# Optimization experiments

Measured on AMD Instinct MI355X. Metric: run time of the kernel, lower is better.

## Reference

```python
import jax, jax.numpy as jnp
import numpy as np

N = 20000; F = 2000; H1 = 256; H2 = 64; E = 320000
BN_EPS = 1e-5


def setup_inputs() -> dict:
    key = jax.random.key(0)
    ks = jax.random.split(key, 32)
    def w(k, shape, fan_in):
        return jax.random.normal(k, shape, jnp.float32) * (1.0 / np.sqrt(fan_in))
    inp = {
        'x': jax.random.normal(ks[0], (N, F), jnp.float32),
        's_src': jax.random.randint(ks[1], (E,), 0, N, jnp.int32),
        's_dst': jax.random.randint(ks[2], (E,), 0, N, jnp.int32),
        's_w': jax.random.uniform(ks[3], (E,), jnp.float32),
        'f_src': jax.random.randint(ks[4], (E,), 0, N, jnp.int32),
        'f_dst': jax.random.randint(ks[5], (E,), 0, N, jnp.int32),
        'f_w': jax.random.uniform(ks[6], (E,), jnp.float32),
        'Ws1': w(ks[7], (F, H1), F), 'bs1': jnp.zeros((H1,), jnp.float32),
        'Ws2': w(ks[8], (H1, H2), H1), 'bs2': jnp.zeros((H2,), jnp.float32),
        'Wf1': w(ks[9], (F, H1), F), 'bf1': jnp.zeros((H1,), jnp.float32),
        'Wf2': w(ks[10], (H1, H2), H1), 'bf2': jnp.zeros((H2,), jnp.float32),
        'Wc1': w(ks[11], (F, H1), F), 'bc1': jnp.zeros((H1,), jnp.float32),
        'Wc2': w(ks[12], (H1, H2), H1), 'bc2': jnp.zeros((H2,), jnp.float32),
        'Wa1': w(ks[13], (H2, 16), H2), 'ba1': jnp.zeros((16,), jnp.float32),
        'Wa2': w(ks[14], (16, 1), 16),
        'Wm': w(ks[15], (H2, H2), H2), 'bm': jnp.zeros((H2,), jnp.float32),
        'Wd': w(ks[16], (H2, H1), H2), 'bd': jnp.zeros((H1,), jnp.float32),
        'bn_g': jnp.ones((H1,), jnp.float32), 'bn_b': jnp.zeros((H1,), jnp.float32),
        'bn_rm': jnp.zeros((H1,), jnp.float32), 'bn_rv': jnp.ones((H1,), jnp.float32),
        'Wpi': w(ks[17], (H1, F), H1), 'bpi': jnp.zeros((F,), jnp.float32),
        'Wdp': w(ks[18], (H1, F), H1), 'bdp': jnp.zeros((F,), jnp.float32),
        'Wmu': w(ks[19], (H1, F), H1), 'bmu': jnp.zeros((F,), jnp.float32),
    }
    return inp


def _spmm(src, dst, ew, h):
    # out[i] = sum over edges (j->i) ew * h[j]   (sparse adj @ dense)
    return jax.ops.segment_sum(h[src] * ew[:, None], dst, num_segments=N)


def _gcn(x, src, dst, ew, W1, b1, W2, b2):
    h = jax.nn.relu(_spmm(src, dst, ew, x @ W1) + b1)
    # dropout p=0 in eval -> identity
    return _spmm(src, dst, ew, h @ W2) + b2


def reference(x, s_src, s_dst, s_w, f_src, f_dst, f_w,
              Ws1, bs1, Ws2, bs2, Wf1, bf1, Wf2, bf2, Wc1, bc1, Wc2, bc2,
              Wa1, ba1, Wa2, Wm, bm, Wd, bd, bn_g, bn_b, bn_rm, bn_rv,
              Wpi, bpi, Wdp, bdp, Wmu, bmu):
    emb1 = _gcn(x, s_src, s_dst, s_w, Ws1, bs1, Ws2, bs2)   # SGCN on sadj
    emb2 = _gcn(x, f_src, f_dst, f_w, Wf1, bf1, Wf2, bf2)   # FGCN on fadj
    # CGCN applied to both graphs (com_comb is computed but unused in original)
    _ = _gcn(x, s_src, s_dst, s_w, Wc1, bc1, Wc2, bc2)
    _ = _gcn(x, f_src, f_dst, f_w, Wc1, bc1, Wc2, bc2)
    z = jnp.stack([emb1, emb2], axis=1)                     # [N, 2, H2]
    att_logits = jnp.tanh(z @ Wa1 + ba1) @ Wa2              # [N, 2, 1]
    beta = jax.nn.softmax(att_logits, axis=1)
    emb = (beta * z).sum(axis=1)                            # [N, H2]
    emb = emb @ Wm + bm                                     # MLP
    # ZINB decoder: Linear -> BatchNorm1d (eval) -> ReLU
    h = emb @ Wd + bd
    h = (h - bn_rm) * jax.lax.rsqrt(bn_rv + BN_EPS) * bn_g + bn_b
    h = jax.nn.relu(h)
    pi = jax.nn.sigmoid(h @ Wpi + bpi)
    disp = jnp.clip(jax.nn.softplus(h @ Wdp + bdp), 1e-4, 1e4)
    mean = jax.nn.sigmoid(h @ Wmu + bmu)
    return (emb1, emb2, emb, pi, disp, mean)
```

## Files before the change

### kernel.cpp

```cpp
#include <hip/hip_runtime.h>


typedef unsigned short bfu;

__device__ __forceinline__ float b2f(bfu u) {
    return __uint_as_float(((unsigned)u) << 16);
}
__device__ __forceinline__ bfu f2b(float f) {
    unsigned u = __float_as_uint(f);
    return (bfu)((u + 0x7FFFu + ((u >> 16) & 1u)) >> 16);
}
__device__ __forceinline__ float ldm(const void* p, size_t i, int bf) {
    return bf ? b2f(((const bfu*)p)[i]) : ((const float*)p)[i];
}
__device__ __forceinline__ void stm(void* p, size_t i, float v, int bf) {
    if (bf) ((bfu*)p)[i] = f2b(v);
    else    ((float*)p)[i] = v;
}

__global__ void detect_dtype_k(const unsigned* __restrict__ sw, int* __restrict__ flag) {
    __shared__ int cnt;
    if (threadIdx.x == 0) cnt = 0;
    __syncthreads();
    unsigned w = sw[threadIdx.x];
    if ((w & 0xFFFFu) >= 0x3F80u) atomicAdd(&cnt, 1);
    __syncthreads();
    if (threadIdx.x == 0) *flag = (cnt < 25) ? 1 : 0;
}

enum { EPI_F32 = 0, EPI_SIG = 1, EPI_SP = 2 };

template <bool AGLB, int EPI>
__global__ __launch_bounds__(256) void gemm_tiled(
    const void* __restrict__ A, const void* __restrict__ B,
    const void* __restrict__ bias,
    float* __restrict__ Cf, void* __restrict__ Cb, size_t cb_off,
    int M, int K, int Nn, const int* __restrict__ flag)
{
    __shared__ __align__(16) float As[16][68];
    __shared__ __align__(16) float Bs[16][68];

    const int bf = *flag;
    const int t = threadIdx.x;
    const int bm0 = blockIdx.x * 64, bn0 = blockIdx.y * 64;
    const int tx = t & 15, ty = t >> 4;

    const int am = t >> 2;
    const int ak = (t & 3) * 4;
    const int gm = bm0 + am;
    const bool arow = gm < M;
    const int bk = t >> 4;
    const int bn = (t & 15) * 4;
    const bool bcol = (bn0 + bn + 3) < Nn;

    float acc[4][4] = {};

    for (int k0 = 0; k0 < K; k0 += 16) {
        float av0 = 0.f, av1 = 0.f, av2 = 0.f, av3 = 0.f;
        float bv0 = 0.f, bv1 = 0.f, bv2 = 0.f, bv3 = 0.f;
        if (arow) {
            size_t off = (size_t)gm * K + k0 + ak;
            if (AGLB && bf) {
                ushort4 v = *(const ushort4*)((const bfu*)A + off);
                av0 = b2f(v.x); av1 = b2f(v.y); av2 = b2f(v.z); av3 = b2f(v.w);
            } else {
                float4 v = *(const float4*)((const float*)A + off);
                av0 = v.x; av1 = v.y; av2 = v.z; av3 = v.w;
            }
        }
        if (bcol) {
            size_t off = (size_t)(k0 + bk) * Nn + bn0 + bn;
            if (bf) {
                ushort4 v = *(const ushort4*)((const bfu*)B + off);
                bv0 = b2f(v.x); bv1 = b2f(v.y); bv2 = b2f(v.z); bv3 = b2f(v.w);
            } else {
                float4 v = *(const float4*)((const float*)B + off);
                bv0 = v.x; bv1 = v.y; bv2 = v.z; bv3 = v.w;
            }
        }

        __syncthreads();
        As[ak + 0][am] = av0; As[ak + 1][am] = av1;
        As[ak + 2][am] = av2; As[ak + 3][am] = av3;
        *(float4*)&Bs[bk][bn] = make_float4(bv0, bv1, bv2, bv3);
        __syncthreads();

        #pragma unroll
        for (int k = 0; k < 16; k++) {
            float4 a4 = *(const float4*)&As[k][ty * 4];
            float4 b4 = *(const float4*)&Bs[k][tx * 4];
            float aa[4] = {a4.x, a4.y, a4.z, a4.w};
            float bb[4] = {b4.x, b4.y, b4.z, b4.w};
            #pragma unroll
            for (int i = 0; i < 4; i++)
                #pragma unroll
                for (int j = 0; j < 4; j++)
                    acc[i][j] += aa[i] * bb[j];
        }
    }

    #pragma unroll
    for (int i = 0; i < 4; i++) {
        int row = bm0 + ty * 4 + i;
        if (row >= M) continue;
        #pragma unroll
        for (int j = 0; j < 4; j++) {
            int col = bn0 + tx * 4 + j;
            if (col >= Nn) continue;
            float v = acc[i][j];
            if constexpr (EPI == EPI_F32) {
                Cf[(size_t)row * Nn + col] = v;
            } else if constexpr (EPI == EPI_SIG) {
                v += ldm(bias, col, bf);
                v = 1.f / (1.f + __expf(-v));
                stm(Cb, cb_off + (size_t)row * Nn + col, v, bf);
            } else {
                v += ldm(bias, col, bf);
                float sp = (v > 20.f) ? v : log1pf(__expf(v));
                sp = fminf(fmaxf(sp, 1e-4f), 1e4f);
                stm(Cb, cb_off + (size_t)row * Nn + col, sp, bf);
            }
        }
    }
}

__global__ __launch_bounds__(256) void spmm_scatter(
    const float* __restrict__ Hin, const int* __restrict__ src,
    const int* __restrict__ dst, const void* __restrict__ w,
    float* __restrict__ outp, int E, int C, const int* __restrict__ flag)
{
    int bf = *flag;
    int gw = (blockIdx.x * 256 + threadIdx.x) >> 6;
    int lane = threadIdx.x & 63;
    if (gw >= E) return;
    int s = src[gw], d = dst[gw];
    float ww = ldm(w, gw, bf);
    const float* hp = Hin + (size_t)s * C;
    float* op = outp + (size_t)d * C;
    for (int c = lane; c < C; c += 64)
        atomicAdd(&op[c], ww * hp[c]);
}

__global__ __launch_bounds__(256) void bias_relu_k(
    float* __restrict__ H, const void* __restrict__ bias, int total, int Cm1,
    const int* __restrict__ flag)
{
    int bf = *flag;
    int i = blockIdx.x * 256 + threadIdx.x;
    if (i >= total) return;
    float v = H[i] + ldm(bias, i & Cm1, bf);
    H[i] = fmaxf(v, 0.f);
}

__global__ __launch_bounds__(256) void bias_store_emb_k(
    float* __restrict__ Ef, const void* __restrict__ bias,
    void* __restrict__ outb, size_t out_off, int total,
    const int* __restrict__ flag)
{
    int bf = *flag;
    int i = blockIdx.x * 256 + threadIdx.x;
    if (i >= total) return;
    float v = Ef[i] + ldm(bias, i & 63, bf);
    Ef[i] = v;
    stm(outb, out_off + i, v, bf);
}

__global__ __launch_bounds__(256) void bn_relu_k(
    float* __restrict__ H, const void* __restrict__ bd,
    const void* __restrict__ g, const void* __restrict__ b,
    const void* __restrict__ rm, const void* __restrict__ rv, int total,
    const int* __restrict__ flag)
{
    int bf = *flag;
    int i = blockIdx.x * 256 + threadIdx.x;
    if (i >= total) return;
    int c = i & 255;
    float v = H[i] + ldm(bd, c, bf);
    v = (v - ldm(rm, c, bf)) * rsqrtf(ldm(rv, c, bf) + 1e-5f) * ldm(g, c, bf)
        + ldm(b, c, bf);
    H[i] = fmaxf(v, 0.f);
}

__global__ __launch_bounds__(256) void attn_mlp_k(
    const float* __restrict__ E1, const float* __restrict__ E2,
    const void* __restrict__ Wa1, const void* __restrict__ ba1,
    const void* __restrict__ Wa2,
    const void* __restrict__ Wm, const void* __restrict__ bm,
    float* __restrict__ Eout, void* __restrict__ outb, size_t out_off,
    const int* __restrict__ flag)
{
    __shared__ float sh[4][3][64];
    int bf = *flag;
    int wid = threadIdx.x >> 6, lane = threadIdx.x & 63;
    int node = blockIdx.x * 4 + wid;

    float e1 = E1[(size_t)node * 64 + lane];
    float e2 = E2[(size_t)node * 64 + lane];
    sh[wid][0][lane] = e1;
    sh[wid][1][lane] = e2;
    __syncthreads();

    float part = 0.f;
    if (lane < 32) {
        int tt = lane & 15;
        const float* es = sh[wid][lane >> 4];
        float a = 0.f;
        for (int m = 0; m < 64; m++) a += es[m] * ldm(Wa1, m * 16 + tt, bf);
        part = tanhf(a + ldm(ba1, tt, bf)) * ldm(Wa2, tt, bf);
    }
    part += __shfl_xor(part, 1);
    part += __shfl_xor(part, 2);
    part += __shfl_xor(part, 4);
    part += __shfl_xor(part, 8);
    float lg1 = __shfl(part, 0);
    float lg2 = __shfl(part, 16);
    float mx = fmaxf(lg1, lg2);
    float p1 = __expf(lg1 - mx), p2 = __expf(lg2 - mx);
    float inv = 1.f / (p1 + p2);
    float comb = (p1 * inv) * e1 + (p2 * inv) * e2;
    sh[wid][2][lane] = comb;
    __syncthreads();

    const float* cs = sh[wid][2];
    float acc = ldm(bm, lane, bf);
    for (int m = 0; m < 64; m++) acc += cs[m] * ldm(Wm, m * 64 + lane, bf);
    size_t idx = (size_t)node * 64 + lane;
    Eout[idx] = acc;
    stm(outb, out_off + idx, acc, bf);
}

extern "C" void kernel_launch(void* const* d_in, const int* in_sizes, int n_in,
                              void* d_out, int out_size, void* d_ws, size_t ws_size,
                              hipStream_t stream)
{
    const int N = 20000, F = 2000, H1 = 256, H2 = 64, E = 320000, FOUT = 2000;

    const void* x     = d_in[0];
    const int* s_src = (const int*)d_in[1];
    const int* s_dst = (const int*)d_in[2];
    const void* s_w   = d_in[3];
    const int* f_src = (const int*)d_in[4];
    const int* f_dst = (const int*)d_in[5];
    const void* f_w   = d_in[6];
    const void *Ws1 = d_in[7],  *bs1 = d_in[8];
    const void *Ws2 = d_in[9],  *bs2 = d_in[10];
    const void *Wf1 = d_in[11], *bf1 = d_in[12];
    const void *Wf2 = d_in[13], *bf2 = d_in[14];
    const void *Wa1 = d_in[19], *ba1 = d_in[20];
    const void *Wa2 = d_in[21];
    const void *Wm  = d_in[22], *bm  = d_in[23];
    const void *Wd  = d_in[24], *bd  = d_in[25];
    const void *bn_g = d_in[26], *bn_b = d_in[27];
    const void *bn_rm = d_in[28], *bn_rv = d_in[29];
    const void *Wpi = d_in[30], *bpi = d_in[31];
    const void *Wdp = d_in[32], *bdp = d_in[33];
    const void *Wmu = d_in[34], *bmu = d_in[35];

    const size_t o_emb1 = 0;
    const size_t o_emb2 = (size_t)N * H2;
    const size_t o_emb  = 2 * (size_t)N * H2;
    const size_t o_pi   = 3 * (size_t)N * H2;
    const size_t o_disp = o_pi + (size_t)N * FOUT;
    const size_t o_mean = o_disp + (size_t)N * FOUT;

    char* wsb = (char*)d_ws;
    int* flag = (int*)wsb;
    float* XW  = (float*)(wsb + 256);
    float* H   = XW + (size_t)N * H1;
    float* G2  = H  + (size_t)N * H1;
    float* e1f = G2 + (size_t)N * H2;
    float* e2f = e1f + (size_t)N * H2;
    float* emf = e2f + (size_t)N * H2;
    float* hdec = XW;

    const int MB = (N + 63) / 64;

    detect_dtype_k<<<1, 256, 0, stream>>>((const unsigned*)s_w, flag);

    gemm_tiled<true, EPI_F32><<<dim3(MB, 4), 256, 0, stream>>>(
        x, Ws1, nullptr, XW, nullptr, 0, N, F, H1, flag);
    hipMemsetAsync(H, 0, (size_t)N * H1 * 4, stream);
    spmm_scatter<<<E / 4, 256, 0, stream>>>(XW, s_src, s_dst, s_w, H, E, H1, flag);
    bias_relu_k<<<(N * H1) / 256, 256, 0, stream>>>(H, bs1, N * H1, H1 - 1, flag);
    gemm_tiled<false, EPI_F32><<<dim3(MB, 1), 256, 0, stream>>>(
        H, Ws2, nullptr, G2, nullptr, 0, N, H1, H2, flag);
    hipMemsetAsync(e1f, 0, (size_t)N * H2 * 4, stream);
    spmm_scatter<<<E / 4, 256, 0, stream>>>(G2, s_src, s_dst, s_w, e1f, E, H2, flag);
    bias_store_emb_k<<<(N * H2) / 256, 256, 0, stream>>>(
        e1f, bs2, d_out, o_emb1, N * H2, flag);

    gemm_tiled<true, EPI_F32><<<dim3(MB, 4), 256, 0, stream>>>(
        x, Wf1, nullptr, XW, nullptr, 0, N, F, H1, flag);
    hipMemsetAsync(H, 0, (size_t)N * H1 * 4, stream);
    spmm_scatter<<<E / 4, 256, 0, stream>>>(XW, f_src, f_dst, f_w, H, E, H1, flag);
    bias_relu_k<<<(N * H1) / 256, 256, 0, stream>>>(H, bf1, N * H1, H1 - 1, flag);
    gemm_tiled<false, EPI_F32><<<dim3(MB, 1), 256, 0, stream>>>(
        H, Wf2, nullptr, G2, nullptr, 0, N, H1, H2, flag);
    hipMemsetAsync(e2f, 0, (size_t)N * H2 * 4, stream);
    spmm_scatter<<<E / 4, 256, 0, stream>>>(G2, f_src, f_dst, f_w, e2f, E, H2, flag);
    bias_store_emb_k<<<(N * H2) / 256, 256, 0, stream>>>(
        e2f, bf2, d_out, o_emb2, N * H2, flag);

    attn_mlp_k<<<N / 4, 256, 0, stream>>>(
        e1f, e2f, Wa1, ba1, Wa2, Wm, bm, emf, d_out, o_emb, flag);

    gemm_tiled<false, EPI_F32><<<dim3(MB, 4), 256, 0, stream>>>(
        emf, Wd, nullptr, hdec, nullptr, 0, N, H2, H1, flag);
    bn_relu_k<<<(N * H1) / 256, 256, 0, stream>>>(
        hdec, bd, bn_g, bn_b, bn_rm, bn_rv, N * H1, flag);

    gemm_tiled<false, EPI_SIG><<<dim3(MB, 32), 256, 0, stream>>>(
        hdec, Wpi, bpi, nullptr, d_out, o_pi, N, H1, FOUT, flag);
    gemm_tiled<false, EPI_SP ><<<dim3(MB, 32), 256, 0, stream>>>(
        hdec, Wdp, bdp, nullptr, d_out, o_disp, N, H1, FOUT, flag);
    gemm_tiled<false, EPI_SIG><<<dim3(MB, 32), 256, 0, stream>>>(
        hdec, Wmu, bmu, nullptr, d_out, o_mean, N, H1, FOUT, flag);
}
```

Measured before the change: 2.915 ms.

## Use bf16 MFMA GEMMs for the large projections when inputs are bf16

Adds a bf16 MFMA GEMM kernel (128x128 tiles, 16x16x32 bf16 instructions) with weight transposes, and routes the big x@W1 and decoder output GEMMs through it when the dtype flag says bf16. The old fp32 tiled path is kept but exits early when bf16 is detected. BN/ReLU now also writes a bf16 copy of the decoder hidden layer to feed the MFMA path. The aim is to move the dominant GEMM cost from scalar FMA onto matrix cores, at the cost of extra transpose launches and reuse of workspace buffers.

```diff
diff --git a/kernel.cpp b/kernel.cpp
--- a/kernel.cpp
+++ b/kernel.cpp
@@ -2,6 +2,8 @@
 
 
 typedef unsigned short bfu;
+typedef __bf16 bf16x8 __attribute__((ext_vector_type(8)));
+typedef float  f32x4  __attribute__((ext_vector_type(4)));
 
 __device__ __forceinline__ float b2f(bfu u) {
     return __uint_as_float(((unsigned)u) << 16);
@@ -30,7 +32,119 @@
 
 enum { EPI_F32 = 0, EPI_SIG = 1, EPI_SP = 2 };
 
-template <bool AGLB, int EPI>
+__global__ __launch_bounds__(256) void transpose_bf16_k(
+    const bfu* __restrict__ in, bfu* __restrict__ out, int R, int C,
+    const int* __restrict__ flag)
+{
+    if (!*flag) return;
+    __shared__ bfu tile[64][66];
+    int r0 = blockIdx.x * 64, c0 = blockIdx.y * 64;
+    int tx = threadIdx.x & 63, ty = threadIdx.x >> 6;
+    for (int i = ty; i < 64; i += 4) {
+        int r = r0 + i, c = c0 + tx;
+        tile[i][tx] = (r < R && c < C) ? in[(size_t)r * C + c] : (bfu)0;
+    }
+    __syncthreads();
+    for (int i = ty; i < 64; i += 4) {
+        int c = c0 + i, r = r0 + tx;
+        if (c < C && r < R) out[(size_t)c * R + r] = tile[tx][i];
+    }
+}
+
+template <int EPI>
+__global__ __launch_bounds__(256) void gemm_mfma(
+    const bfu* __restrict__ A, const bfu* __restrict__ Bt,
+    const void* __restrict__ bias,
+    float* __restrict__ Cf, void* __restrict__ Cb, size_t cb_off,
+    int M, int K, int Nn, const int* __restrict__ flag)
+{
+    if (!*flag) return;
+    __shared__ __align__(16) bfu As[128 * 72];
+    __shared__ __align__(16) bfu Bs[128 * 72];
+
+    const int t = threadIdx.x;
+    const int bm0 = blockIdx.x * 128, bn0 = blockIdx.y * 128;
+    const int lane = t & 63, wid = t >> 6;
+    const int wm = (wid >> 1) * 64, wn = (wid & 1) * 64;
+    const int lr = lane & 15;
+    const int lk = (lane >> 4) * 8;
+    const int lq = (lane >> 4) * 4;
+
+    f32x4 acc[4][4] = {};
+
+    const int srow = t >> 3;
+    const int skoff = (t & 7) * 8;
+
+    for (int k0 = 0; k0 < K; k0 += 64) {
+        int4 va[4], vb[4];
+        #pragma unroll
+        for (int h = 0; h < 4; h++) {
+            int row = srow + h * 32;
+            int gk = k0 + skoff;
+            va[h] = make_int4(0, 0, 0, 0);
+            vb[h] = make_int4(0, 0, 0, 0);
+            int gm = bm0 + row;
+            if (gm < M && gk < K)
+                va[h] = *(const int4*)(A + (size_t)gm * K + gk);
+            int gn = bn0 + row;
+            if (gn < Nn && gk < K)
+                vb[h] = *(const int4*)(Bt + (size_t)gn * K + gk);
+        }
+        __syncthreads();
+        #pragma unroll
+        for (int h = 0; h < 4; h++) {
+            int row = srow + h * 32;
+            *(int4*)&As[row * 72 + skoff] = va[h];
+            *(int4*)&Bs[row * 72 + skoff] = vb[h];
+        }
+        __syncthreads();
+
+        #pragma unroll
+        for (int kk = 0; kk < 2; kk++) {
+            bf16x8 af[4], bq[4];
+            #pragma unroll
+            for (int i = 0; i < 4; i++) {
+                af[i] = *(const bf16x8*)&As[(wm + i * 16 + lr) * 72 + kk * 32 + lk];
+                bq[i] = *(const bf16x8*)&Bs[(wn + i * 16 + lr) * 72 + kk * 32 + lk];
+            }
+            #pragma unroll
+            for (int i = 0; i < 4; i++)
+                #pragma unroll
+                for (int j = 0; j < 4; j++)
+                    acc[i][j] = __builtin_amdgcn_mfma_f32_16x16x32_bf16(
+                        af[i], bq[j], acc[i][j], 0, 0, 0);
+        }
+    }
+
+    #pragma unroll
+    for (int j = 0; j < 4; j++) {
+        int col = bn0 + wn + j * 16 + lr;
+        if (col >= Nn) continue;
+        #pragma unroll
+        for (int i = 0; i < 4; i++) {
+            #pragma unroll
+            for (int r = 0; r < 4; r++) {
+                int row = bm0 + wm + i * 16 + lq + r;
+                if (row >= M) continue;
+                float v = acc[i][j][r];
+                if constexpr (EPI == EPI_F32) {
+                    Cf[(size_t)row * Nn + col] = v;
+                } else if constexpr (EPI == EPI_SIG) {
+                    v += ldm(bias, col, 1);
+                    v = 1.f / (1.f + __expf(-v));
+                    stm(Cb, cb_off + (size_t)row * Nn + col, v, 1);
+                } else {
+                    v += ldm(bias, col, 1);
+                    float sp = (v > 20.f) ? v : log1pf(__expf(v));
+                    sp = fminf(fmaxf(sp, 1e-4f), 1e4f);
+                    stm(Cb, cb_off + (size_t)row * Nn + col, sp, 1);
+                }
+            }
+        }
+    }
+}
+
+template <bool AGLB, int EPI, bool FP32ONLY>
 __global__ __launch_bounds__(256) void gemm_tiled(
     const void* __restrict__ A, const void* __restrict__ B,
     const void* __restrict__ bias,
@@ -41,6 +155,7 @@
     __shared__ __align__(16) float Bs[16][68];
 
     const int bf = *flag;
+    if (FP32ONLY && bf) return;
     const int t = threadIdx.x;
     const int bm0 = blockIdx.x * 64, bn0 = blockIdx.y * 64;
     const int tx = t & 15, ty = t >> 4;
@@ -168,8 +283,8 @@
 __global__ __launch_bounds__(256) void bn_relu_k(
     float* __restrict__ H, const void* __restrict__ bd,
     const void* __restrict__ g, const void* __restrict__ b,
-    const void* __restrict__ rm, const void* __restrict__ rv, int total,
-    const int* __restrict__ flag)
+    const void* __restrict__ rm, const void* __restrict__ rv,
+    bfu* __restrict__ hb, int total, const int* __restrict__ flag)
 {
     int bf = *flag;
     int i = blockIdx.x * 256 + threadIdx.x;
@@ -178,7 +293,9 @@
     float v = H[i] + ldm(bd, c, bf);
     v = (v - ldm(rm, c, bf)) * rsqrtf(ldm(rv, c, bf) + 1e-5f) * ldm(g, c, bf)
         + ldm(b, c, bf);
-    H[i] = fmaxf(v, 0.f);
+    v = fmaxf(v, 0.f);
+    H[i] = v;
+    if (bf) hb[i] = f2b(v);
 }
 
 __global__ __launch_bounds__(256) void attn_mlp_k(
@@ -272,29 +389,40 @@
     float* e2f = e1f + (size_t)N * H2;
     float* emf = e2f + (size_t)N * H2;
     float* hdec = XW;
-
-    const int MB = (N + 63) / 64;
+    bfu* hdec_bf = (bfu*)H;
+    bfu* Bt      = (bfu*)G2;
+
+    const int MB  = (N + 63) / 64;
+    const int MB2 = (N + 127) / 128;
 
     detect_dtype_k<<<1, 256, 0, stream>>>((const unsigned*)s_w, flag);
 
-    gemm_tiled<true, EPI_F32><<<dim3(MB, 4), 256, 0, stream>>>(
+    transpose_bf16_k<<<dim3(32, 4), 256, 0, stream>>>(
+        (const bfu*)Ws1, Bt, F, H1, flag);
+    gemm_mfma<EPI_F32><<<dim3(MB2, 2), 256, 0, stream>>>(
+        (const bfu*)x, Bt, nullptr, XW, nullptr, 0, N, F, H1, flag);
+    gemm_tiled<true, EPI_F32, true><<<dim3(MB, 4), 256, 0, stream>>>(
         x, Ws1, nullptr, XW, nullptr, 0, N, F, H1, flag);
     hipMemsetAsync(H, 0, (size_t)N * H1 * 4, stream);
     spmm_scatter<<<E / 4, 256, 0, stream>>>(XW, s_src, s_dst, s_w, H, E, H1, flag);
     bias_relu_k<<<(N * H1) / 256, 256, 0, stream>>>(H, bs1, N * H1, H1 - 1, flag);
-    gemm_tiled<false, EPI_F32><<<dim3(MB, 1), 256, 0, stream>>>(
+    gemm_tiled<false, EPI_F32, false><<<dim3(MB, 1), 256, 0, stream>>>(
         H, Ws2, nullptr, G2, nullptr, 0, N, H1, H2, flag);
     hipMemsetAsync(e1f, 0, (size_t)N * H2 * 4, stream);
     spmm_scatter<<<E / 4, 256, 0, stream>>>(G2, s_src, s_dst, s_w, e1f, E, H2, flag);
     bias_store_emb_k<<<(N * H2) / 256, 256, 0, stream>>>(
         e1f, bs2, d_out, o_emb1, N * H2, flag);
 
-    gemm_tiled<true, EPI_F32><<<dim3(MB, 4), 256, 0, stream>>>(
+    transpose_bf16_k<<<dim3(32, 4), 256, 0, stream>>>(
+        (const bfu*)Wf1, Bt, F, H1, flag);
+    gemm_mfma<EPI_F32><<<dim3(MB2, 2), 256, 0, stream>>>(
+        (const bfu*)x, Bt, nullptr, XW, nullptr, 0, N, F, H1, flag);
+    gemm_tiled<true, EPI_F32, true><<<dim3(MB, 4), 256, 0, stream>>>(
         x, Wf1, nullptr, XW, nullptr, 0, N, F, H1, flag);
     hipMemsetAsync(H, 0, (size_t)N * H1 * 4, stream);
     spmm_scatter<<<E / 4, 256, 0, stream>>>(XW, f_src, f_dst, f_w, H, E, H1, flag);
     bias_relu_k<<<(N * H1) / 256, 256, 0, stream>>>(H, bf1, N * H1, H1 - 1, flag);
-    gemm_tiled<false, EPI_F32><<<dim3(MB, 1), 256, 0, stream>>>(
+    gemm_tiled<false, EPI_F32, false><<<dim3(MB, 1), 256, 0, stream>>>(
         H, Wf2, nullptr, G2, nullptr, 0, N, H1, H2, flag);
     hipMemsetAsync(e2f, 0, (size_t)N * H2 * 4, stream);
     spmm_scatter<<<E / 4, 256, 0, stream>>>(G2, f_src, f_dst, f_w, e2f, E, H2, flag);
@@ -304,15 +432,27 @@
     attn_mlp_k<<<N / 4, 256, 0, stream>>>(
         e1f, e2f, Wa1, ba1, Wa2, Wm, bm, emf, d_out, o_emb, flag);
 
-    gemm_tiled<false, EPI_F32><<<dim3(MB, 4), 256, 0, stream>>>(
+    gemm_tiled<false, EPI_F32, false><<<dim3(MB, 4), 256, 0, stream>>>(
         emf, Wd, nullptr, hdec, nullptr, 0, N, H2, H1, flag);
     bn_relu_k<<<(N * H1) / 256, 256, 0, stream>>>(
-        hdec, bd, bn_g, bn_b, bn_rm, bn_rv, N * H1, flag);
-
-    gemm_tiled<false, EPI_SIG><<<dim3(MB, 32), 256, 0, stream>>>(
+        hdec, bd, bn_g, bn_b, bn_rm, bn_rv, hdec_bf, N * H1, flag);
+
+    transpose_bf16_k<<<dim3(4, 32), 256, 0, stream>>>(
+        (const bfu*)Wpi, Bt, H1, FOUT, flag);
+    gemm_mfma<EPI_SIG><<<dim3(MB2, 16), 256, 0, stream>>>(
+        hdec_bf, Bt, bpi, nullptr, d_out, o_pi, N, H1, FOUT, flag);
+    gemm_tiled<false, EPI_SIG, true><<<dim3(MB, 32), 256, 0, stream>>>(
         hdec, Wpi, bpi, nullptr, d_out, o_pi, N, H1, FOUT, flag);
-    gemm_tiled<false, EPI_SP ><<<dim3(MB, 32), 256, 0, stream>>>(
+    transpose_bf16_k<<<dim3(4, 32), 256, 0, stream>>>(
+        (const bfu*)Wdp, Bt, H1, FOUT, flag);
+    gemm_mfma<EPI_SP><<<dim3(MB2, 16), 256, 0, stream>>>(
+        hdec_bf, Bt, bdp, nullptr, d_out, o_disp, N, H1, FOUT, flag);
+    gemm_tiled<false, EPI_SP, true><<<dim3(MB, 32), 256, 0, stream>>>(
         hdec, Wdp, bdp, nullptr, d_out, o_disp, N, H1, FOUT, flag);
-    gemm_tiled<false, EPI_SIG><<<dim3(MB, 32), 256, 0, stream>>>(
+    transpose_bf16_k<<<dim3(4, 32), 256, 0, stream>>>(
+        (const bfu*)Wmu, Bt, H1, FOUT, flag);
+    gemm_mfma<EPI_SIG><<<dim3(MB2, 16), 256, 0, stream>>>(
+        hdec_bf, Bt, bmu, nullptr, d_out, o_mean, N, H1, FOUT, flag);
+    gemm_tiled<false, EPI_SIG, true><<<dim3(MB, 32), 256, 0, stream>>>(
         hdec, Wmu, bmu, nullptr, d_out, o_mean, N, H1, FOUT, flag);
 }
```

Measured after the change: 2.852 ms. 1.02x faster.
